# Performance work log

Measured on AMD Instinct MI355X. Metric: run time of the kernel, lower is better.

## Reference

```python
import jax, jax.numpy as jnp
import numpy as np

B, C, M = 2048, 1, 80  # M = max_object; matrices are (M+1)x(M+1)


def setup_inputs() -> dict:
    key = jax.random.key(0)
    k1, k2, k3, k4 = jax.random.split(key, 4)
    inp = {
        "input": jax.random.normal(k1, (B, C, M + 1, M + 1), dtype=jnp.float32),
        "target": jax.random.randint(k2, (B, C, M + 1, M + 1), 0, 2, dtype=jnp.int32),
        "mask0": jax.random.randint(k3, (B, C, M + 1), 0, 2, dtype=jnp.int32),
        "mask1": jax.random.randint(k4, (B, C, M + 1), 0, 2, dtype=jnp.int32),
        "outputs": 0,
        "current_fair_labels": 0,
        "next_fair_labels": 0,
    }
    return inp


def reference(input, target, mask0, mask1, outputs, current_fair_labels, next_fair_labels):
    f32 = jnp.float32
    m0 = mask0.astype(f32)[:, :, :, None]   # [B,C,M+1,1] (row mask, broadcast over cols)
    m1 = mask1.astype(f32)[:, :, None, :]   # [B,C,1,M+1] (col mask, broadcast over rows)
    mask_region = m0 * m1                    # [B,C,M+1,M+1]
    mask_region_pre = mask_region.at[:, :, M, :].set(0.0)   # zero last row
    mask_region_next = mask_region.at[:, :, :, M].set(0.0)  # zero last col
    mask_region_union = mask_region_pre * mask_region_next

    input_pre = jax.nn.softmax(mask_region_pre * input, axis=3)
    input_next = jax.nn.softmax(mask_region_next * input, axis=2)
    input_all = input_pre.at[:, :, :M, :M].set(
        jnp.maximum(input_pre, input_next)[:, :, :M, :M])

    t = target.astype(jnp.bool_).astype(f32)
    target_pre = mask_region_pre * t
    target_next = mask_region_next * t
    target_union = mask_region_union * t

    target_num = t.sum()
    n_pre = target_pre.sum()
    n_next = target_next.sum()
    n_union = target_union.sum()

    s_pre = -(target_pre * jnp.log(input_pre)).sum()
    loss_pre = jnp.where(n_pre > 0, s_pre / n_pre, s_pre)

    s_next = -(target_next * jnp.log(input_next)).sum()
    loss_next = jnp.where(n_next > 0, s_next / n_next, s_next)

    s_all = -(target_pre * jnp.log(input_all)).sum()
    loss = jnp.where((n_pre > 0) & (n_next > 0), s_all / n_pre, s_all)

    # |1 - p_pre - (1 - p_next)| == |p_next - p_pre|
    s_sim = (target_union * jnp.abs(input_next - input_pre)).sum()
    loss_similarity = jnp.where(n_union > 0, s_sim / target_num, s_sim)

    # accuracy on "pre" direction (argmax over cols, drop last row)
    idx_t_pre = jnp.argmax(target_pre, axis=3)[:, :, :-1]
    indexes_pre = jnp.argmax(input_all, axis=3)[:, :, :-1]
    mpre = mask0.astype(f32)[:, :, :-1]
    n_mpre = mpre.sum()
    s_acc_pre = ((indexes_pre == idx_t_pre).astype(f32) * mpre).sum()
    accuracy_pre = jnp.where(n_mpre > 0, s_acc_pre / n_mpre, s_acc_pre + 1.0)

    # accuracy on "next" direction (argmax over rows, drop last col)
    idx_t_next = jnp.argmax(target_next, axis=2)[:, :, :-1]
    indexes_next = jnp.argmax(input_next, axis=2)[:, :, :-1]
    mnext = mask1.astype(f32)[:, :, :-1]
    n_mnext = mnext.sum()
    s_acc_next = ((indexes_next == idx_t_next).astype(f32) * mnext).sum()
    accuracy_next = jnp.where(n_mnext > 0, s_acc_next / n_mnext, s_acc_next + 1.0)

    total = (loss_pre + loss_next + loss + loss_similarity) / 4.0
    return (loss_pre, loss_next, loss_similarity, total,
            accuracy_pre, accuracy_next, (accuracy_pre + accuracy_next) / 2.0,
            indexes_pre)
```

## Files before the change

### kernel.cpp

```cpp
#include <hip/hip_runtime.h>

#define M1 81
#define MSZ 80
#define NEL (M1 * M1)
#define NTW ((NEL + 31) / 32)
#define NACC 12


__device__ __forceinline__ float tbitf(const unsigned* tb, int idx) {
    return (float)((tb[idx >> 5] >> (idx & 31)) & 1u);
}

__global__ __launch_bounds__(256) void sst_main(
    const float* __restrict__ input,
    const int* __restrict__ target,
    const int* __restrict__ mask0,
    const int* __restrict__ mask1,
    float* __restrict__ out_idx,
    float* __restrict__ part,
    int slices)
{
    __shared__ float s_x[NEL];
    __shared__ unsigned s_tb[NTW];
    __shared__ float s_m0[M1], s_m1[M1];
    __shared__ float2 s_rowc[M1];
    __shared__ float4 s_colc[M1];
    __shared__ float s_pa[243];
    __shared__ float s_pv[243];
    __shared__ unsigned char s_pi[243];
    __shared__ unsigned char s_pt[243];
    __shared__ float s_accf[NACC];

    const int tid = threadIdx.x;
    const int slice = blockIdx.x;
    const size_t base = (size_t)slice * NEL;

    if (tid < NACC) s_accf[tid] = 0.0f;
    if (tid < M1) s_m0[tid] = (float)mask0[slice * M1 + tid];
    else if (tid >= 128 && tid < 128 + M1) s_m1[tid - 128] = (float)mask1[slice * M1 + (tid - 128)];

    for (int i = tid; i < NEL; i += 256) {
        s_x[i] = input[base + i];
        unsigned long long m = __ballot(target[base + i] != 0);
        if ((tid & 63) == 0) {
            int w = (i >> 5) & ~1;
            s_tb[w] = (unsigned)m;
            if (w + 1 < NTW) s_tb[w + 1] = (unsigned)(m >> 32);
        }
    }
    __syncthreads();

    float a[NACC];
#pragma unroll
    for (int k = 0; k < NACC; ++k) a[k] = 0.0f;

    const int g  = tid / 3;
    const int j  = tid - 3 * g;
    const int c0 = j * 27;
    const bool act = (tid < 243);

    if (act) {
        const int r = g;
        const float m0p = (r == MSZ) ? 0.0f : s_m0[r];
        const int rb = r * M1;
        float rs = 0.0f;
        for (int i = 0; i < 27; ++i) {
            const int c = c0 + i;
            rs += __expf(m0p * s_m1[c] * s_x[rb + c]);
        }
        s_pa[tid] = rs;
    }
    __syncthreads();
    if (tid < M1) {
        const float rsum = s_pa[3 * tid] + s_pa[3 * tid + 1] + s_pa[3 * tid + 2];
        s_rowc[tid] = make_float2(__logf(rsum), 1.0f / rsum);
    }
    __syncthreads();

    if (act) {
        const int c = g;
        const float mcol = (c == MSZ) ? 0.0f : s_m1[c];
        float cs = 0.0f, best = -1.0f;
        int bidx = c0, tIdxn = 127;
        for (int i = 0; i < 27; ++i) {
            const int r = c0 + i;
            const float mn = mcol * s_m0[r];
            const float e = __expf(mn * s_x[r * M1 + c]);
            cs += e;
            if (e > best) { best = e; bidx = r; }
            const float tn = tbitf(s_tb, r * M1 + c) * mn;
            if (tn != 0.0f && tIdxn == 127) tIdxn = r;
        }
        s_pa[tid] = cs;
        s_pv[tid] = best;
        s_pi[tid] = (unsigned char)bidx;
        s_pt[tid] = (unsigned char)tIdxn;
    }
    __syncthreads();
    if (tid < M1) {
        const int c = tid;
        const float csum = s_pa[3 * c] + s_pa[3 * c + 1] + s_pa[3 * c + 2];
        s_colc[c] = make_float4(s_m1[c], __logf(csum), 1.0f / csum, 0.0f);
        if (c < MSZ) {
            float bv = s_pv[3 * c]; int bi = s_pi[3 * c];
            float v1 = s_pv[3 * c + 1]; if (v1 > bv) { bv = v1; bi = s_pi[3 * c + 1]; }
            float v2 = s_pv[3 * c + 2]; if (v2 > bv) { bv = v2; bi = s_pi[3 * c + 2]; }
            int ti = min(min((int)s_pt[3 * c], (int)s_pt[3 * c + 1]), (int)s_pt[3 * c + 2]);
            if (ti == 127) ti = 0;
            const float m1c = s_m1[c];
            a[9]  += (bi == ti) ? m1c : 0.0f;
            a[11] += m1c;
        }
    }
    __syncthreads();

    if (act) {
        const int r = g;
        const int rb = r * M1;
        const float m0f = s_m0[r];
        const float m0p = (r == MSZ) ? 0.0f : m0f;
        const float2 rc = s_rowc[r];
        const float lr = rc.x, invr = rc.y;
        float bbest = -3.402823466e38f;
        int bbidx = c0, tIdx = 127;
        const int cend = (j == 2) ? MSZ : (c0 + 27);
        for (int c = c0; c < cend; ++c) {
            const float4 cc = s_colc[c];
            const float m1c = cc.x, kc = cc.y, invc = cc.z;
            const float x = s_x[rb + c];
            const float t = tbitf(s_tb, rb + c);
            const float mf = m0f * m1c;
            const float mp = m0p * m1c;
            const float z = mf * x;
            const float tp = t * mp;
            const float tn = t * mf;
            a[0] += t;
            a[1] += tp;
            a[2] += tn;
            a[3] += tp;
            a[4] = fmaf(tp, lr - z, a[4]);
            a[5] = fmaf(tn, kc - z, a[5]);
            const float mlk = fminf(lr, kc);
            a[6] = fmaf(tp, mlk - z, a[6]);
            const float e = __expf(z);
            a[7] = fmaf(tp * e, fabsf(invc - invr), a[7]);
            const float val = z - mlk;
            if (val > bbest) { bbest = val; bbidx = c; }
            if (tp != 0.0f && tIdx == 127) tIdx = c;
        }
        if (j == 2) {
            const int c = MSZ;
            const float m1c = s_m1[c];
            const float x = s_x[rb + c];
            const float t = tbitf(s_tb, rb + c);
            const float mp = m0p * m1c;
            const float zp = mp * x;
            const float tp = t * mp;
            a[0] += t;
            a[1] += tp;
            a[4] = fmaf(tp, lr - zp, a[4]);
            a[6] = fmaf(tp, lr - zp, a[6]);
            const float val = zp - lr;
            if (val > bbest) { bbest = val; bbidx = c; }
            if (tp != 0.0f && tIdx == 127) tIdx = c;
        }
        s_pv[tid] = bbest;
        s_pi[tid] = (unsigned char)bbidx;
        s_pt[tid] = (unsigned char)tIdx;
    }
    __syncthreads();

    if (tid < MSZ) {
        const int r = tid;
        float bv = s_pv[3 * r]; int bi = s_pi[3 * r];
        float v1 = s_pv[3 * r + 1]; if (v1 > bv) { bv = v1; bi = s_pi[3 * r + 1]; }
        float v2 = s_pv[3 * r + 2]; if (v2 > bv) { bv = v2; bi = s_pi[3 * r + 2]; }
        int ti = min(min((int)s_pt[3 * r], (int)s_pt[3 * r + 1]), (int)s_pt[3 * r + 2]);
        if (ti == 127) ti = 0;
        out_idx[(size_t)slice * MSZ + r] = (float)bi;
        const float m0r = s_m0[r];
        a[8]  += (bi == ti) ? m0r : 0.0f;
        a[10] += m0r;
    }

#pragma unroll
    for (int k = 0; k < NACC; ++k) {
        float v = a[k];
        for (int off = 32; off > 0; off >>= 1) v += __shfl_down(v, off);
        if ((tid & 63) == 0) atomicAdd(&s_accf[k], v);
    }
    __syncthreads();
    if (tid < NACC) part[(size_t)tid * slices + slice] = s_accf[tid];
}

__global__ __launch_bounds__(256) void sst_final(
    const float* __restrict__ part, int slices, float* __restrict__ out)
{
    __shared__ double s_part[4][NACC];
    const int tid = threadIdx.x;
    double l[NACC];
#pragma unroll
    for (int k = 0; k < NACC; ++k) l[k] = 0.0;
    for (int s = tid; s < slices; s += 256) {
#pragma unroll
        for (int k = 0; k < NACC; ++k) l[k] += (double)part[(size_t)k * slices + s];
    }
#pragma unroll
    for (int k = 0; k < NACC; ++k) {
        double v = l[k];
        for (int off = 32; off > 0; off >>= 1) v += __shfl_down(v, off);
        if ((tid & 63) == 0) s_part[tid >> 6][k] = v;
    }
    __syncthreads();
    if (tid == 0) {
        double g[NACC];
#pragma unroll
        for (int k = 0; k < NACC; ++k)
            g[k] = s_part[0][k] + s_part[1][k] + s_part[2][k] + s_part[3][k];
        const double tnum = g[0], npre = g[1], nnext = g[2], nunion = g[3];
        const double spre = g[4], snext = g[5], sall = g[6], ssim = g[7];
        const double accp = g[8], accn = g[9], nmp = g[10], nmn = g[11];
        const double loss_pre  = (npre > 0.0) ? spre / npre : spre;
        const double loss_next = (nnext > 0.0) ? snext / nnext : snext;
        const double loss      = (npre > 0.0 && nnext > 0.0) ? sall / npre : sall;
        const double loss_sim  = (nunion > 0.0) ? ssim / tnum : ssim;
        const double total = (loss_pre + loss_next + loss + loss_sim) * 0.25;
        const double ap = (nmp > 0.0) ? accp / nmp : accp + 1.0;
        const double an = (nmn > 0.0) ? accn / nmn : accn + 1.0;
        out[0] = (float)loss_pre;
        out[1] = (float)loss_next;
        out[2] = (float)loss_sim;
        out[3] = (float)total;
        out[4] = (float)ap;
        out[5] = (float)an;
        out[6] = (float)((ap + an) * 0.5);
    }
}

extern "C" void kernel_launch(void* const* d_in, const int* in_sizes, int n_in,
                              void* d_out, int out_size, void* d_ws, size_t ws_size,
                              hipStream_t stream) {
    const float* input  = (const float*)d_in[0];
    const int*   target = (const int*)d_in[1];
    const int*   mask0  = (const int*)d_in[2];
    const int*   mask1  = (const int*)d_in[3];
    float* out = (float*)d_out;
    float* part = (float*)d_ws;

    const int slices = in_sizes[0] / NEL;

    sst_main<<<slices, 256, 0, stream>>>(input, target, mask0, mask1, out + 7, part, slices);
    sst_final<<<1, 256, 0, stream>>>(part, slices, out);
}
```

Baseline: 183.3 us.

## Map rows to wavefronts with lane-per-column, reading global memory directly instead of staging in LDS

The per-slice kernel no longer stages the 81x81 input tile and a target bitmask in shared memory. Each wavefront now walks rows and each lane owns a column (two passes over global memory). Column softmax sums and argmaxes are kept in registers per lane, row sums are taken with wave shuffles, and the first-target row/column search uses ballots. This removes the LDS staging, the strided 3-threads-per-row layout and several barriers. In exchange input is read from global twice, lanes 17-63 sit idle in the second column chunk, and per-row shuffle reductions are added.

```diff
diff --git a/kernel.cpp b/kernel.cpp
--- a/kernel.cpp
+++ b/kernel.cpp
@@ -3,13 +3,9 @@
 #define M1 81
 #define MSZ 80
 #define NEL (M1 * M1)
-#define NTW ((NEL + 31) / 32)
 #define NACC 12
-
-
-__device__ __forceinline__ float tbitf(const unsigned* tb, int idx) {
-    return (float)((tb[idx >> 5] >> (idx & 31)) & 1u);
-}
+#define BIGKC 1.0e30f
+
 
 __global__ __launch_bounds__(256) void sst_main(
     const float* __restrict__ input,
@@ -20,174 +16,199 @@
     float* __restrict__ part,
     int slices)
 {
-    __shared__ float s_x[NEL];
-    __shared__ unsigned s_tb[NTW];
-    __shared__ float s_m0[M1], s_m1[M1];
-    __shared__ float2 s_rowc[M1];
-    __shared__ float4 s_colc[M1];
-    __shared__ float s_pa[243];
-    __shared__ float s_pv[243];
-    __shared__ unsigned char s_pi[243];
-    __shared__ unsigned char s_pt[243];
-    __shared__ float s_accf[NACC];
-
-    const int tid = threadIdx.x;
+    __shared__ float  s_m0[M1];
+    __shared__ float2 s_row[M1];
+    __shared__ float2 s_col[M1];
+    __shared__ float  s_cs[4][M1];
+    __shared__ float  s_cv[4][M1];
+    __shared__ int    s_ci[4][M1];
+    __shared__ int    s_ct[4][M1];
+    __shared__ float  s_accf[NACC];
+
+    const int tid   = threadIdx.x;
+    const int lane  = tid & 63;
+    const int w     = tid >> 6;
     const int slice = blockIdx.x;
     const size_t base = (size_t)slice * NEL;
 
     if (tid < NACC) s_accf[tid] = 0.0f;
     if (tid < M1) s_m0[tid] = (float)mask0[slice * M1 + tid];
-    else if (tid >= 128 && tid < 128 + M1) s_m1[tid - 128] = (float)mask1[slice * M1 + (tid - 128)];
-
-    for (int i = tid; i < NEL; i += 256) {
-        s_x[i] = input[base + i];
-        unsigned long long m = __ballot(target[base + i] != 0);
-        if ((tid & 63) == 0) {
-            int w = (i >> 5) & ~1;
-            s_tb[w] = (unsigned)m;
-            if (w + 1 < NTW) s_tb[w + 1] = (unsigned)(m >> 32);
-        }
-    }
-    __syncthreads();
+
+    const float m1c1 = (float)mask1[slice * M1 + lane];
+    float m1c2 = 0.0f;
+    if (lane < 17) m1c2 = (float)mask1[slice * M1 + 64 + lane];
+    const float m1n2 = (lane == 16) ? 0.0f : m1c2;
 
     float a[NACC];
 #pragma unroll
     for (int k = 0; k < NACC; ++k) a[k] = 0.0f;
 
-    const int g  = tid / 3;
-    const int j  = tid - 3 * g;
-    const int c0 = j * 27;
-    const bool act = (tid < 243);
-
-    if (act) {
-        const int r = g;
-        const float m0p = (r == MSZ) ? 0.0f : s_m0[r];
-        const int rb = r * M1;
-        float rs = 0.0f;
-        for (int i = 0; i < 27; ++i) {
-            const int c = c0 + i;
-            rs += __expf(m0p * s_m1[c] * s_x[rb + c]);
-        }
-        s_pa[tid] = rs;
-    }
-    __syncthreads();
-    if (tid < M1) {
-        const float rsum = s_pa[3 * tid] + s_pa[3 * tid + 1] + s_pa[3 * tid + 2];
-        s_rowc[tid] = make_float2(__logf(rsum), 1.0f / rsum);
-    }
-    __syncthreads();
-
-    if (act) {
-        const int c = g;
-        const float mcol = (c == MSZ) ? 0.0f : s_m1[c];
-        float cs = 0.0f, best = -1.0f;
-        int bidx = c0, tIdxn = 127;
-        for (int i = 0; i < 27; ++i) {
-            const int r = c0 + i;
-            const float mn = mcol * s_m0[r];
-            const float e = __expf(mn * s_x[r * M1 + c]);
-            cs += e;
-            if (e > best) { best = e; bidx = r; }
-            const float tn = tbitf(s_tb, r * M1 + c) * mn;
-            if (tn != 0.0f && tIdxn == 127) tIdxn = r;
-        }
-        s_pa[tid] = cs;
-        s_pv[tid] = best;
-        s_pi[tid] = (unsigned char)bidx;
-        s_pt[tid] = (unsigned char)tIdxn;
-    }
-    __syncthreads();
+    __syncthreads();
+
+    float csum1 = 0.0f, csum2 = 0.0f;
+    float cmv1 = -1.0f, cmv2 = -1.0f;
+    int   cmi1 = 0,     cmi2 = 0;
+
+    for (int r = w; r < M1; r += 4) {
+        const float m0f = s_m0[r];
+        const size_t rb = base + (size_t)r * M1;
+        const float x1 = input[rb + lane];
+        float x2 = 0.0f;
+        if (lane < 17) x2 = input[rb + 64 + lane];
+
+        if (r < MSZ) {
+            const float e1 = __expf(m0f * m1c1 * x1);
+            float e2 = 0.0f;
+            if (lane < 17) e2 = __expf(m0f * m1c2 * x2);
+            csum1 += e1;
+            if (e1 > cmv1) { cmv1 = e1; cmi1 = r; }
+            if (lane < 16) {
+                csum2 += e2;
+                if (e2 > cmv2) { cmv2 = e2; cmi2 = r; }
+            }
+            float s = e1 + e2;
+#pragma unroll
+            for (int off = 1; off < 64; off <<= 1) s += __shfl_xor(s, off);
+            if (lane == 0) s_row[r] = make_float2(__logf(s), 1.0f / s);
+        } else {
+            const float e1 = __expf(m0f * m1c1 * x1);
+            csum1 += e1;
+            if (e1 > cmv1) { cmv1 = e1; cmi1 = MSZ; }
+            if (lane < 16) {
+                const float e2 = __expf(m0f * m1c2 * x2);
+                csum2 += e2;
+                if (e2 > cmv2) { cmv2 = e2; cmi2 = MSZ; }
+            }
+            if (lane == 0) s_row[MSZ] = make_float2(__logf(81.0f), 1.0f / 81.0f);
+        }
+    }
+    s_cs[w][lane] = csum1;
+    s_cv[w][lane] = cmv1;
+    s_ci[w][lane] = cmi1;
+    if (lane < 16) {
+        s_cs[w][64 + lane] = csum2;
+        s_cv[w][64 + lane] = cmv2;
+        s_ci[w][64 + lane] = cmi2;
+    }
+    __syncthreads();
+
     if (tid < M1) {
         const int c = tid;
-        const float csum = s_pa[3 * c] + s_pa[3 * c + 1] + s_pa[3 * c + 2];
-        s_colc[c] = make_float4(s_m1[c], __logf(csum), 1.0f / csum, 0.0f);
         if (c < MSZ) {
-            float bv = s_pv[3 * c]; int bi = s_pi[3 * c];
-            float v1 = s_pv[3 * c + 1]; if (v1 > bv) { bv = v1; bi = s_pi[3 * c + 1]; }
-            float v2 = s_pv[3 * c + 2]; if (v2 > bv) { bv = v2; bi = s_pi[3 * c + 2]; }
-            int ti = min(min((int)s_pt[3 * c], (int)s_pt[3 * c + 1]), (int)s_pt[3 * c + 2]);
-            if (ti == 127) ti = 0;
-            const float m1c = s_m1[c];
-            a[9]  += (bi == ti) ? m1c : 0.0f;
-            a[11] += m1c;
-        }
-    }
-    __syncthreads();
-
-    if (act) {
-        const int r = g;
-        const int rb = r * M1;
+            const float csum = s_cs[0][c] + s_cs[1][c] + s_cs[2][c] + s_cs[3][c];
+            float bv = s_cv[0][c]; int bi = s_ci[0][c];
+#pragma unroll
+            for (int ww = 1; ww < 4; ++ww) {
+                const float v = s_cv[ww][c]; const int i = s_ci[ww][c];
+                if (v > bv || (v == bv && i < bi)) { bv = v; bi = i; }
+            }
+            s_ci[0][c] = bi;
+            s_col[c] = make_float2(__logf(csum), 1.0f / csum);
+        } else {
+            s_col[MSZ] = make_float2(BIGKC, 1.0f / 81.0f);
+        }
+    }
+    __syncthreads();
+
+    const float2 cc1 = s_col[lane];
+    const float kc1 = cc1.x, invc1 = cc1.y;
+    float kc2 = 0.0f, invc2 = 0.0f;
+    if (lane < 17) { const float2 cc2 = s_col[64 + lane]; kc2 = cc2.x; invc2 = cc2.y; }
+
+    int ct1 = 127, ct2 = 127;
+
+    for (int r = w; r < M1; r += 4) {
         const float m0f = s_m0[r];
-        const float m0p = (r == MSZ) ? 0.0f : m0f;
-        const float2 rc = s_rowc[r];
-        const float lr = rc.x, invr = rc.y;
-        float bbest = -3.402823466e38f;
-        int bbidx = c0, tIdx = 127;
-        const int cend = (j == 2) ? MSZ : (c0 + 27);
-        for (int c = c0; c < cend; ++c) {
-            const float4 cc = s_colc[c];
-            const float m1c = cc.x, kc = cc.y, invc = cc.z;
-            const float x = s_x[rb + c];
-            const float t = tbitf(s_tb, rb + c);
-            const float mf = m0f * m1c;
-            const float mp = m0p * m1c;
-            const float z = mf * x;
-            const float tp = t * mp;
-            const float tn = t * mf;
-            a[0] += t;
-            a[1] += tp;
-            a[2] += tn;
-            a[3] += tp;
-            a[4] = fmaf(tp, lr - z, a[4]);
-            a[5] = fmaf(tn, kc - z, a[5]);
-            const float mlk = fminf(lr, kc);
-            a[6] = fmaf(tp, mlk - z, a[6]);
-            const float e = __expf(z);
-            a[7] = fmaf(tp * e, fabsf(invc - invr), a[7]);
-            const float val = z - mlk;
-            if (val > bbest) { bbest = val; bbidx = c; }
-            if (tp != 0.0f && tIdx == 127) tIdx = c;
-        }
-        if (j == 2) {
-            const int c = MSZ;
-            const float m1c = s_m1[c];
-            const float x = s_x[rb + c];
-            const float t = tbitf(s_tb, rb + c);
-            const float mp = m0p * m1c;
-            const float zp = mp * x;
-            const float tp = t * mp;
-            a[0] += t;
-            a[1] += tp;
-            a[4] = fmaf(tp, lr - zp, a[4]);
-            a[6] = fmaf(tp, lr - zp, a[6]);
-            const float val = zp - lr;
-            if (val > bbest) { bbest = val; bbidx = c; }
-            if (tp != 0.0f && tIdx == 127) tIdx = c;
-        }
-        s_pv[tid] = bbest;
-        s_pi[tid] = (unsigned char)bbidx;
-        s_pt[tid] = (unsigned char)tIdx;
-    }
+        const bool last = (r == MSZ);
+        const float m0p = last ? 0.0f : m0f;
+        const float2 rw = s_row[r];
+        const float lr = rw.x, invr = rw.y;
+        const size_t rb = base + (size_t)r * M1;
+
+        const float x1 = input[rb + lane];
+        const int   t1 = target[rb + lane];
+        float x2 = 0.0f; int t2 = 0;
+        if (lane < 17) { x2 = input[rb + 64 + lane]; t2 = target[rb + 64 + lane]; }
+
+        const float tf1 = (t1 != 0) ? 1.0f : 0.0f;
+        const float mf1 = m0f * m1c1;
+        const float z1  = mf1 * x1;
+        const float mp1 = m0p * m1c1;
+        const float tp1 = tf1 * mp1;
+        const float tn1 = tf1 * mf1;
+        a[0] += tf1; a[1] += tp1; a[2] += tn1; a[3] += tp1;
+        a[4] = fmaf(tp1, lr - z1, a[4]);
+        a[5] = fmaf(tn1, kc1 - z1, a[5]);
+        const float mlk1 = fminf(lr, kc1);
+        a[6] = fmaf(tp1, mlk1 - z1, a[6]);
+        const float e1 = __expf(z1);
+        a[7] = fmaf(tp1 * e1, fabsf(invc1 - invr), a[7]);
+        float bv = z1 - mlk1; int bi = lane;
+        const bool tpnz1 = (tp1 != 0.0f);
+        if (tn1 != 0.0f && ct1 == 127) ct1 = r;
+
+        float val2 = -3.402823466e38f;
+        bool tpnz2 = false;
+        if (lane < 17) {
+            const float tf2 = (t2 != 0) ? 1.0f : 0.0f;
+            const float mf2 = m0f * m1c2;
+            const float z2  = mf2 * x2;
+            const float mp2 = m0p * m1c2;
+            const float tp2 = tf2 * mp2;
+            const float tn2 = tf2 * (m0f * m1n2);
+            const float tun2 = (lane == 16) ? 0.0f : tp2;
+            a[0] += tf2; a[1] += tp2; a[2] += tn2; a[3] += tun2;
+            a[4] = fmaf(tp2, lr - z2, a[4]);
+            a[5] = fmaf(tn2, kc2 - z2, a[5]);
+            const float mlk2 = fminf(lr, kc2);
+            a[6] = fmaf(tp2, mlk2 - z2, a[6]);
+            const float e2 = __expf(z2);
+            a[7] = fmaf(tun2 * e2, fabsf(invc2 - invr), a[7]);
+            val2 = z2 - mlk2;
+            tpnz2 = (tp2 != 0.0f);
+            if (tn2 != 0.0f && ct2 == 127) ct2 = r;
+        }
+
+        if (!last) {
+            if (val2 > bv) { bv = val2; bi = 64 + lane; }
+#pragma unroll
+            for (int off = 32; off > 0; off >>= 1) {
+                const float v2 = __shfl_down(bv, off);
+                const int   i2 = __shfl_down(bi, off);
+                if (v2 > bv || (v2 == bv && i2 < bi)) { bv = v2; bi = i2; }
+            }
+            const unsigned long long b1 = __ballot(tpnz1);
+            const unsigned long long b2 = __ballot(tpnz2);
+            if (lane == 0) {
+                int ti = 0;
+                if (b1) ti = __ffsll((long long)b1) - 1;
+                else if (b2) ti = 64 + __ffsll((long long)b2) - 1;
+                out_idx[(size_t)slice * MSZ + r] = (float)bi;
+                a[8]  += (bi == ti) ? m0f : 0.0f;
+                a[10] += m0f;
+            }
+        }
+    }
+
+    s_ct[w][lane] = ct1;
+    if (lane < 16) s_ct[w][64 + lane] = ct2;
     __syncthreads();
 
     if (tid < MSZ) {
-        const int r = tid;
-        float bv = s_pv[3 * r]; int bi = s_pi[3 * r];
-        float v1 = s_pv[3 * r + 1]; if (v1 > bv) { bv = v1; bi = s_pi[3 * r + 1]; }
-        float v2 = s_pv[3 * r + 2]; if (v2 > bv) { bv = v2; bi = s_pi[3 * r + 2]; }
-        int ti = min(min((int)s_pt[3 * r], (int)s_pt[3 * r + 1]), (int)s_pt[3 * r + 2]);
+        const int c = tid;
+        int ti = min(min(s_ct[0][c], s_ct[1][c]), min(s_ct[2][c], s_ct[3][c]));
         if (ti == 127) ti = 0;
-        out_idx[(size_t)slice * MSZ + r] = (float)bi;
-        const float m0r = s_m0[r];
-        a[8]  += (bi == ti) ? m0r : 0.0f;
-        a[10] += m0r;
+        const int bi = s_ci[0][c];
+        const float m1c = (float)mask1[slice * M1 + c];
+        a[9]  += (bi == ti) ? m1c : 0.0f;
+        a[11] += m1c;
     }
 
 #pragma unroll
     for (int k = 0; k < NACC; ++k) {
         float v = a[k];
         for (int off = 32; off > 0; off >>= 1) v += __shfl_down(v, off);
-        if ((tid & 63) == 0) atomicAdd(&s_accf[k], v);
+        if (lane == 0) atomicAdd(&s_accf[k], v);
     }
     __syncthreads();
     if (tid < NACC) part[(size_t)tid * slices + slice] = s_accf[tid];
```

After: 224.8 us. 22.6% more time.

## Split per-slice kernel into row/column stats and elementwise kernels with quad threads

Applied to the files above, without the earlier changes.

Replaces the one-block-per-slice kernel, which staged the input and a target bitmask in shared memory, with two grid-wide kernels. The first kernel computes row and column softmax statistics, the column argmax and the column target index, using four threads per row or column combined with cross-lane shuffles, and stores them in workspace. The second kernel does the elementwise loss and row argmax work. Both kernels read global memory directly and write per-block partial sums that the final kernel reduces. The aim is higher occupancy and more parallelism than the serial shared-memory phases allowed. The cost is reading input and target several times from global memory, with partly uncoalesced per-thread row segments.

```diff
diff --git a/kernel.cpp b/kernel.cpp
--- a/kernel.cpp
+++ b/kernel.cpp
@@ -3,141 +3,157 @@
 #define M1 81
 #define MSZ 80
 #define NEL (M1 * M1)
-#define NTW ((NEL + 31) / 32)
 #define NACC 12
-
-
-__device__ __forceinline__ float tbitf(const unsigned* tb, int idx) {
-    return (float)((tb[idx >> 5] >> (idx & 31)) & 1u);
-}
-
-__global__ __launch_bounds__(256) void sst_main(
+#define BIGKC 1.0e30f
+
+
+
+__device__ __forceinline__ void block_reduce_write(
+    float* a, float* part, int nbTot, int slot)
+{
+    __shared__ float s_wv[4][NACC];
+    const int tid = threadIdx.x;
+    const int lane = tid & 63, w = tid >> 6;
+#pragma unroll
+    for (int k = 0; k < NACC; ++k) {
+        float v = a[k];
+        for (int off = 32; off > 0; off >>= 1) v += __shfl_down(v, off);
+        if (lane == 0) s_wv[w][k] = v;
+    }
+    __syncthreads();
+    if (tid < NACC) {
+        part[tid * nbTot + slot] =
+            s_wv[0][tid] + s_wv[1][tid] + s_wv[2][tid] + s_wv[3][tid];
+    }
+}
+
+__global__ __launch_bounds__(256) void sst_stats(
     const float* __restrict__ input,
     const int* __restrict__ target,
     const int* __restrict__ mask0,
     const int* __restrict__ mask1,
+    float2* __restrict__ rowc,
+    float4* __restrict__ colc,
+    float* __restrict__ part, int nbTot, int slices, int rowBlocks)
+{
+    const int tid = threadIdx.x;
+    float a[NACC];
+#pragma unroll
+    for (int k = 0; k < NACC; ++k) a[k] = 0.0f;
+
+    if ((int)blockIdx.x < rowBlocks) {
+        const int t = blockIdx.x * 256 + tid;
+        if (t < slices * 324) {
+            const int slice = t / 324;
+            const int rem = t - slice * 324;
+            const int r = rem >> 2;
+            const int q = rem & 3;
+            const int mbase = slice * M1;
+            if (r == MSZ) {
+                if (q == 0) rowc[mbase + r] = make_float2(__logf(81.0f), 1.0f / 81.0f);
+            } else {
+                const float m0 = (float)mask0[mbase + r];
+                const size_t rb = (size_t)slice * NEL + (size_t)r * M1;
+                const int c0 = (q == 0) ? 0 : (20 * q + 1);
+                const int c1 = (q == 3) ? M1 : ((q == 0) ? 21 : c0 + 20);
+                float s = 0.0f;
+                for (int c = c0; c < c1; ++c) {
+                    const float m1c = (float)mask1[mbase + c];
+                    s += __expf(m0 * m1c * input[rb + c]);
+                }
+                s += __shfl_xor(s, 1);
+                s += __shfl_xor(s, 2);
+                if (q == 0) rowc[mbase + r] = make_float2(__logf(s), 1.0f / s);
+            }
+        }
+        return;
+    }
+
+    const int t = (blockIdx.x - rowBlocks) * 256 + tid;
+    if (t < slices * 324) {
+        const int slice = t / 324;
+        const int rem = t - slice * 324;
+        const int c = rem >> 2;
+        const int q = rem & 3;
+        const int mbase = slice * M1;
+        if (c == MSZ) {
+            if (q == 0) colc[mbase + c] =
+                make_float4((float)mask1[mbase + c], BIGKC, 1.0f / 81.0f, 0.0f);
+        } else {
+            const float m1c = (float)mask1[mbase + c];
+            const size_t sb = (size_t)slice * NEL;
+            const int r0 = (q == 0) ? 0 : (20 * q + 1);
+            const int r1 = (q == 0) ? 21 : (r0 + 20);
+            float cs = 0.0f, bv = -1.0f;
+            int bi = r0, ct = 127;
+            for (int r = r0; r < r1; ++r) {
+                const float m0r = (float)mask0[mbase + r];
+                const float mn = m1c * m0r;
+                const float e = __expf(mn * input[sb + (size_t)r * M1 + c]);
+                cs += e;
+                if (e > bv) { bv = e; bi = r; }
+                if (ct == 127 && mn != 0.0f && target[sb + (size_t)r * M1 + c] != 0) ct = r;
+            }
+            cs += __shfl_xor(cs, 1);
+            cs += __shfl_xor(cs, 2);
+            float ov = __shfl_xor(bv, 1); int oi = __shfl_xor(bi, 1); int ot = __shfl_xor(ct, 1);
+            if (ov > bv || (ov == bv && oi < bi)) { bv = ov; bi = oi; }
+            ct = min(ct, ot);
+            ov = __shfl_xor(bv, 2); oi = __shfl_xor(bi, 2); ot = __shfl_xor(ct, 2);
+            if (ov > bv || (ov == bv && oi < bi)) { bv = ov; bi = oi; }
+            ct = min(ct, ot);
+            if (q == 0) {
+                colc[mbase + c] = make_float4(m1c, __logf(cs), 1.0f / cs, 0.0f);
+                const int ti = (ct == 127) ? 0 : ct;
+                a[9]  += (bi == ti) ? m1c : 0.0f;
+                a[11] += m1c;
+            }
+        }
+    }
+    block_reduce_write(a, part, nbTot, blockIdx.x - rowBlocks);
+}
+
+__global__ __launch_bounds__(256) void sst_elem(
+    const float* __restrict__ input,
+    const int* __restrict__ target,
+    const int* __restrict__ mask0,
+    const float2* __restrict__ rowc,
+    const float4* __restrict__ colc,
     float* __restrict__ out_idx,
-    float* __restrict__ part,
-    int slices)
-{
-    __shared__ float s_x[NEL];
-    __shared__ unsigned s_tb[NTW];
-    __shared__ float s_m0[M1], s_m1[M1];
-    __shared__ float2 s_rowc[M1];
-    __shared__ float4 s_colc[M1];
-    __shared__ float s_pa[243];
-    __shared__ float s_pv[243];
-    __shared__ unsigned char s_pi[243];
-    __shared__ unsigned char s_pt[243];
-    __shared__ float s_accf[NACC];
-
-    const int tid = threadIdx.x;
-    const int slice = blockIdx.x;
-    const size_t base = (size_t)slice * NEL;
-
-    if (tid < NACC) s_accf[tid] = 0.0f;
-    if (tid < M1) s_m0[tid] = (float)mask0[slice * M1 + tid];
-    else if (tid >= 128 && tid < 128 + M1) s_m1[tid - 128] = (float)mask1[slice * M1 + (tid - 128)];
-
-    for (int i = tid; i < NEL; i += 256) {
-        s_x[i] = input[base + i];
-        unsigned long long m = __ballot(target[base + i] != 0);
-        if ((tid & 63) == 0) {
-            int w = (i >> 5) & ~1;
-            s_tb[w] = (unsigned)m;
-            if (w + 1 < NTW) s_tb[w + 1] = (unsigned)(m >> 32);
-        }
-    }
-    __syncthreads();
-
+    float* __restrict__ part, int nbTot, int partBase, int slices)
+{
+    const int tid = threadIdx.x;
     float a[NACC];
 #pragma unroll
     for (int k = 0; k < NACC; ++k) a[k] = 0.0f;
 
-    const int g  = tid / 3;
-    const int j  = tid - 3 * g;
-    const int c0 = j * 27;
-    const bool act = (tid < 243);
-
-    if (act) {
-        const int r = g;
-        const float m0p = (r == MSZ) ? 0.0f : s_m0[r];
-        const int rb = r * M1;
-        float rs = 0.0f;
-        for (int i = 0; i < 27; ++i) {
-            const int c = c0 + i;
-            rs += __expf(m0p * s_m1[c] * s_x[rb + c]);
-        }
-        s_pa[tid] = rs;
-    }
-    __syncthreads();
-    if (tid < M1) {
-        const float rsum = s_pa[3 * tid] + s_pa[3 * tid + 1] + s_pa[3 * tid + 2];
-        s_rowc[tid] = make_float2(__logf(rsum), 1.0f / rsum);
-    }
-    __syncthreads();
-
-    if (act) {
-        const int c = g;
-        const float mcol = (c == MSZ) ? 0.0f : s_m1[c];
-        float cs = 0.0f, best = -1.0f;
-        int bidx = c0, tIdxn = 127;
-        for (int i = 0; i < 27; ++i) {
-            const int r = c0 + i;
-            const float mn = mcol * s_m0[r];
-            const float e = __expf(mn * s_x[r * M1 + c]);
-            cs += e;
-            if (e > best) { best = e; bidx = r; }
-            const float tn = tbitf(s_tb, r * M1 + c) * mn;
-            if (tn != 0.0f && tIdxn == 127) tIdxn = r;
-        }
-        s_pa[tid] = cs;
-        s_pv[tid] = best;
-        s_pi[tid] = (unsigned char)bidx;
-        s_pt[tid] = (unsigned char)tIdxn;
-    }
-    __syncthreads();
-    if (tid < M1) {
-        const int c = tid;
-        const float csum = s_pa[3 * c] + s_pa[3 * c + 1] + s_pa[3 * c + 2];
-        s_colc[c] = make_float4(s_m1[c], __logf(csum), 1.0f / csum, 0.0f);
-        if (c < MSZ) {
-            float bv = s_pv[3 * c]; int bi = s_pi[3 * c];
-            float v1 = s_pv[3 * c + 1]; if (v1 > bv) { bv = v1; bi = s_pi[3 * c + 1]; }
-            float v2 = s_pv[3 * c + 2]; if (v2 > bv) { bv = v2; bi = s_pi[3 * c + 2]; }
-            int ti = min(min((int)s_pt[3 * c], (int)s_pt[3 * c + 1]), (int)s_pt[3 * c + 2]);
-            if (ti == 127) ti = 0;
-            const float m1c = s_m1[c];
-            a[9]  += (bi == ti) ? m1c : 0.0f;
-            a[11] += m1c;
-        }
-    }
-    __syncthreads();
-
-    if (act) {
-        const int r = g;
-        const int rb = r * M1;
-        const float m0f = s_m0[r];
+    const int t = blockIdx.x * 256 + tid;
+    if (t < slices * 324) {
+        const int slice = t / 324;
+        const int rem = t - slice * 324;
+        const int r = rem >> 2;
+        const int q = rem & 3;
+        const int mbase = slice * M1;
+        const size_t rb = (size_t)slice * NEL + (size_t)r * M1;
+        const float m0f = (float)mask0[mbase + r];
         const float m0p = (r == MSZ) ? 0.0f : m0f;
-        const float2 rc = s_rowc[r];
-        const float lr = rc.x, invr = rc.y;
-        float bbest = -3.402823466e38f;
-        int bbidx = c0, tIdx = 127;
-        const int cend = (j == 2) ? MSZ : (c0 + 27);
-        for (int c = c0; c < cend; ++c) {
-            const float4 cc = s_colc[c];
+        const float2 rw = rowc[mbase + r];
+        const float lr = rw.x, invr = rw.y;
+        const int c0 = (q == 0) ? 0 : (20 * q + 1);
+        const int c1 = (q == 3) ? MSZ : ((q == 0) ? 21 : c0 + 20);
+        float bv = -3.402823466e38f;
+        int bi = c0, ti = 127;
+        for (int c = c0; c < c1; ++c) {
+            const float4 cc = colc[mbase + c];
             const float m1c = cc.x, kc = cc.y, invc = cc.z;
-            const float x = s_x[rb + c];
-            const float t = tbitf(s_tb, rb + c);
+            const float x = input[rb + c];
+            const float tf = (target[rb + c] != 0) ? 1.0f : 0.0f;
             const float mf = m0f * m1c;
+            const float z  = mf * x;
             const float mp = m0p * m1c;
-            const float z = mf * x;
-            const float tp = t * mp;
-            const float tn = t * mf;
-            a[0] += t;
-            a[1] += tp;
-            a[2] += tn;
-            a[3] += tp;
+            const float tp = tf * mp;
+            const float tn = tf * mf;
+            a[0] += tf; a[1] += tp; a[2] += tn; a[3] += tp;
             a[4] = fmaf(tp, lr - z, a[4]);
             a[5] = fmaf(tn, kc - z, a[5]);
             const float mlk = fminf(lr, kc);
@@ -145,65 +161,50 @@
             const float e = __expf(z);
             a[7] = fmaf(tp * e, fabsf(invc - invr), a[7]);
             const float val = z - mlk;
-            if (val > bbest) { bbest = val; bbidx = c; }
-            if (tp != 0.0f && tIdx == 127) tIdx = c;
-        }
-        if (j == 2) {
-            const int c = MSZ;
-            const float m1c = s_m1[c];
-            const float x = s_x[rb + c];
-            const float t = tbitf(s_tb, rb + c);
-            const float mp = m0p * m1c;
-            const float zp = mp * x;
-            const float tp = t * mp;
-            a[0] += t;
-            a[1] += tp;
-            a[4] = fmaf(tp, lr - zp, a[4]);
-            a[6] = fmaf(tp, lr - zp, a[6]);
-            const float val = zp - lr;
-            if (val > bbest) { bbest = val; bbidx = c; }
-            if (tp != 0.0f && tIdx == 127) tIdx = c;
-        }
-        s_pv[tid] = bbest;
-        s_pi[tid] = (unsigned char)bbidx;
-        s_pt[tid] = (unsigned char)tIdx;
-    }
-    __syncthreads();
-
-    if (tid < MSZ) {
-        const int r = tid;
-        float bv = s_pv[3 * r]; int bi = s_pi[3 * r];
-        float v1 = s_pv[3 * r + 1]; if (v1 > bv) { bv = v1; bi = s_pi[3 * r + 1]; }
-        float v2 = s_pv[3 * r + 2]; if (v2 > bv) { bv = v2; bi = s_pi[3 * r + 2]; }
-        int ti = min(min((int)s_pt[3 * r], (int)s_pt[3 * r + 1]), (int)s_pt[3 * r + 2]);
-        if (ti == 127) ti = 0;
-        out_idx[(size_t)slice * MSZ + r] = (float)bi;
-        const float m0r = s_m0[r];
-        a[8]  += (bi == ti) ? m0r : 0.0f;
-        a[10] += m0r;
-    }
-
-#pragma unroll
-    for (int k = 0; k < NACC; ++k) {
-        float v = a[k];
-        for (int off = 32; off > 0; off >>= 1) v += __shfl_down(v, off);
-        if ((tid & 63) == 0) atomicAdd(&s_accf[k], v);
-    }
-    __syncthreads();
-    if (tid < NACC) part[(size_t)tid * slices + slice] = s_accf[tid];
+            if (val > bv) { bv = val; bi = c; }
+            if (ti == 127 && tp != 0.0f) ti = c;
+        }
+        if (q == 3) {
+            const float4 cc = colc[mbase + MSZ];
+            const float m1c = cc.x;
+            const float x = input[rb + MSZ];
+            const float tf = (target[rb + MSZ] != 0) ? 1.0f : 0.0f;
+            const float z  = m0f * m1c * x;
+            const float tp = tf * (m0p * m1c);
+            a[0] += tf; a[1] += tp;
+            a[4] = fmaf(tp, lr - z, a[4]);
+            a[6] = fmaf(tp, lr - z, a[6]);
+            const float val = z - lr;
+            if (val > bv) { bv = val; bi = MSZ; }
+            if (ti == 127 && tp != 0.0f) ti = MSZ;
+        }
+        float ov = __shfl_xor(bv, 1); int oi = __shfl_xor(bi, 1); int ot = __shfl_xor(ti, 1);
+        if (ov > bv || (ov == bv && oi < bi)) { bv = ov; bi = oi; }
+        ti = min(ti, ot);
+        ov = __shfl_xor(bv, 2); oi = __shfl_xor(bi, 2); ot = __shfl_xor(ti, 2);
+        if (ov > bv || (ov == bv && oi < bi)) { bv = ov; bi = oi; }
+        ti = min(ti, ot);
+        if (q == 0 && r < MSZ) {
+            out_idx[(size_t)slice * MSZ + r] = (float)bi;
+            const int tm = (ti == 127) ? 0 : ti;
+            a[8]  += (bi == tm) ? m0f : 0.0f;
+            a[10] += m0f;
+        }
+    }
+    block_reduce_write(a, part, nbTot, partBase + blockIdx.x);
 }
 
 __global__ __launch_bounds__(256) void sst_final(
-    const float* __restrict__ part, int slices, float* __restrict__ out)
+    const float* __restrict__ part, int nbTot, float* __restrict__ out)
 {
     __shared__ double s_part[4][NACC];
     const int tid = threadIdx.x;
     double l[NACC];
 #pragma unroll
     for (int k = 0; k < NACC; ++k) l[k] = 0.0;
-    for (int s = tid; s < slices; s += 256) {
-#pragma unroll
-        for (int k = 0; k < NACC; ++k) l[k] += (double)part[(size_t)k * slices + s];
+    for (int s = tid; s < nbTot; s += 256) {
+#pragma unroll
+        for (int k = 0; k < NACC; ++k) l[k] += (double)part[(size_t)k * nbTot + s];
     }
 #pragma unroll
     for (int k = 0; k < NACC; ++k) {
@@ -245,10 +246,19 @@
     const int*   mask0  = (const int*)d_in[2];
     const int*   mask1  = (const int*)d_in[3];
     float* out = (float*)d_out;
-    float* part = (float*)d_ws;
 
     const int slices = in_sizes[0] / NEL;
-
-    sst_main<<<slices, 256, 0, stream>>>(input, target, mask0, mask1, out + 7, part, slices);
-    sst_final<<<1, 256, 0, stream>>>(part, slices, out);
-}
+    const int qBlocks = (slices * 324 + 255) / 256;
+    const int k1Blocks = qBlocks * 2;
+    const int nbTot = qBlocks * 2;
+
+    float4* colc = (float4*)d_ws;
+    float2* rowc = (float2*)(colc + (size_t)slices * M1);
+    float*  part = (float*)(rowc + (size_t)slices * M1);
+
+    sst_stats<<<k1Blocks, 256, 0, stream>>>(input, target, mask0, mask1,
+                                            rowc, colc, part, nbTot, slices, qBlocks);
+    sst_elem<<<qBlocks, 256, 0, stream>>>(input, target, mask0,
+                                          rowc, colc, out + 7, part, nbTot, qBlocks, slices);
+    sst_final<<<1, 256, 0, stream>>>(part, nbTot, out);
+}
```

Measured after the change: 313.0 us. +70.8%, slower.

## Run row and column softmax passes concurrently with 512-thread blocks and algebraic loss split

Applied to the files above, without the earlier changes.

Raises the block to 512 threads so the row-sum pass and the column-sum pass run in parallel on separate thread groups instead of in two serialized phases. The log-softmax terms are split algebraically: target-weighted z sums and target counts are accumulated in the first pass and combined with log-sums afterwards, and the target-index searches move into that pass. The final pass uses six threads per row. Per-wave partials go to a shared array instead of shared atomics. This removes one sync phase and shortens per-thread loops, at the cost of more shared memory, more registers per block, and reordered floating-point sums.

```diff
diff --git a/kernel.cpp b/kernel.cpp
--- a/kernel.cpp
+++ b/kernel.cpp
@@ -5,13 +5,16 @@
 #define NEL (M1 * M1)
 #define NTW ((NEL + 31) / 32)
 #define NACC 12
+#define BIGKC 1.0e30f
+#define LOG81 4.394449154672439f
+#define INV81 0.012345679012345678f
 
 
 __device__ __forceinline__ float tbitf(const unsigned* tb, int idx) {
     return (float)((tb[idx >> 5] >> (idx & 31)) & 1u);
 }
 
-__global__ __launch_bounds__(256) void sst_main(
+__global__ __launch_bounds__(512, 8) void sst_main(
     const float* __restrict__ input,
     const int* __restrict__ target,
     const int* __restrict__ mask0,
@@ -25,172 +28,198 @@
     __shared__ float s_m0[M1], s_m1[M1];
     __shared__ float2 s_rowc[M1];
     __shared__ float4 s_colc[M1];
-    __shared__ float s_pa[243];
-    __shared__ float s_pv[243];
-    __shared__ unsigned char s_pi[243];
-    __shared__ unsigned char s_pt[243];
-    __shared__ float s_accf[NACC];
-
-    const int tid = threadIdx.x;
+    __shared__ float s_pA[486];
+    __shared__ float s_pB[486];
+    __shared__ float s_pV[486];
+    __shared__ unsigned char s_pI[486];
+    __shared__ unsigned char s_pT[486];
+    __shared__ unsigned char s_ti[M1];
+    __shared__ float s_wv[8][NACC];
+
+    const int tid   = threadIdx.x;
+    const int lane  = tid & 63;
+    const int w     = tid >> 6;
     const int slice = blockIdx.x;
     const size_t base = (size_t)slice * NEL;
 
-    if (tid < NACC) s_accf[tid] = 0.0f;
     if (tid < M1) s_m0[tid] = (float)mask0[slice * M1 + tid];
     else if (tid >= 128 && tid < 128 + M1) s_m1[tid - 128] = (float)mask1[slice * M1 + (tid - 128)];
 
-    for (int i = tid; i < NEL; i += 256) {
+    float a[NACC];
+#pragma unroll
+    for (int k = 0; k < NACC; ++k) a[k] = 0.0f;
+
+    for (int i = tid; i < NEL; i += 512) {
         s_x[i] = input[base + i];
-        unsigned long long m = __ballot(target[base + i] != 0);
-        if ((tid & 63) == 0) {
-            int w = (i >> 5) & ~1;
-            s_tb[w] = (unsigned)m;
-            if (w + 1 < NTW) s_tb[w + 1] = (unsigned)(m >> 32);
-        }
-    }
-    __syncthreads();
-
-    float a[NACC];
-#pragma unroll
-    for (int k = 0; k < NACC; ++k) a[k] = 0.0f;
-
-    const int g  = tid / 3;
-    const int j  = tid - 3 * g;
-    const int c0 = j * 27;
-    const bool act = (tid < 243);
-
-    if (act) {
-        const int r = g;
-        const float m0p = (r == MSZ) ? 0.0f : s_m0[r];
-        const int rb = r * M1;
-        float rs = 0.0f;
-        for (int i = 0; i < 27; ++i) {
-            const int c = c0 + i;
-            rs += __expf(m0p * s_m1[c] * s_x[rb + c]);
-        }
-        s_pa[tid] = rs;
-    }
-    __syncthreads();
+        const int tv = target[base + i];
+        a[0] += (tv != 0) ? 1.0f : 0.0f;
+        unsigned long long m = __ballot(tv != 0);
+        if (lane == 0) {
+            const int w2 = (i >> 5) & ~1;
+            s_tb[w2] = (unsigned)m;
+            if (w2 + 1 < NTW) s_tb[w2 + 1] = (unsigned)(m >> 32);
+        }
+    }
+    __syncthreads();
+
+    if (tid < 243) {
+        const int r = tid / 3, j = tid - 3 * (tid / 3);
+        if (r < MSZ) {
+            const float m0p = s_m0[r];
+            const int rb = r * M1;
+            const int c0 = 27 * j;
+            float rs = 0.0f, St = 0.0f, Sz = 0.0f;
+            int ti = 127;
+            for (int c = c0; c < c0 + 27; ++c) {
+                const float m1c = s_m1[c];
+                const float x = s_x[rb + c];
+                const float mp = m0p * m1c;
+                const float z = mp * x;
+                rs += __expf(z);
+                const float tf = tbitf(s_tb, rb + c);
+                const float tp = tf * mp;
+                a[1] += tp;
+                a[3] += (c < MSZ) ? tp : 0.0f;
+                Sz = fmaf(tp, z, Sz);
+                St += tp;
+                if (ti == 127 && tp != 0.0f) ti = c;
+            }
+            a[4] -= Sz;
+            a[6] -= Sz;
+            s_pA[tid] = rs;
+            s_pB[tid] = St;
+            s_pT[tid] = (unsigned char)ti;
+        }
+    } else if (tid >= 256 && tid < 499) {
+        const int u = tid - 256;
+        const int c = u / 3, j = u - 3 * (u / 3);
+        if (c < MSZ) {
+            const float m1n = s_m1[c];
+            const int r0 = 27 * j;
+            float cs = 0.0f, Sn = 0.0f, Sz = 0.0f, bv = -1.0f;
+            int bi = r0, ct = 127;
+            for (int r = r0; r < r0 + 27; ++r) {
+                const float mn = m1n * s_m0[r];
+                const float x = s_x[r * M1 + c];
+                const float z = mn * x;
+                const float e = __expf(z);
+                cs += e;
+                if (e > bv) { bv = e; bi = r; }
+                const float tf = tbitf(s_tb, r * M1 + c);
+                const float tn = tf * mn;
+                a[2] += tn;
+                Sz = fmaf(tn, z, Sz);
+                Sn += tn;
+                if (ct == 127 && tn != 0.0f) ct = r;
+            }
+            a[5] -= Sz;
+            s_pA[243 + u] = cs;
+            s_pB[243 + u] = Sn;
+            s_pV[243 + u] = bv;
+            s_pI[243 + u] = (unsigned char)bi;
+            s_pT[243 + u] = (unsigned char)ct;
+        }
+    }
+    __syncthreads();
+
     if (tid < M1) {
-        const float rsum = s_pa[3 * tid] + s_pa[3 * tid + 1] + s_pa[3 * tid + 2];
-        s_rowc[tid] = make_float2(__logf(rsum), 1.0f / rsum);
-    }
-    __syncthreads();
-
-    if (act) {
-        const int c = g;
-        const float mcol = (c == MSZ) ? 0.0f : s_m1[c];
-        float cs = 0.0f, best = -1.0f;
-        int bidx = c0, tIdxn = 127;
-        for (int i = 0; i < 27; ++i) {
-            const int r = c0 + i;
-            const float mn = mcol * s_m0[r];
-            const float e = __expf(mn * s_x[r * M1 + c]);
-            cs += e;
-            if (e > best) { best = e; bidx = r; }
-            const float tn = tbitf(s_tb, r * M1 + c) * mn;
-            if (tn != 0.0f && tIdxn == 127) tIdxn = r;
-        }
-        s_pa[tid] = cs;
-        s_pv[tid] = best;
-        s_pi[tid] = (unsigned char)bidx;
-        s_pt[tid] = (unsigned char)tIdxn;
-    }
-    __syncthreads();
-    if (tid < M1) {
-        const int c = tid;
-        const float csum = s_pa[3 * c] + s_pa[3 * c + 1] + s_pa[3 * c + 2];
-        s_colc[c] = make_float4(s_m1[c], __logf(csum), 1.0f / csum, 0.0f);
+        const int r = tid;
+        if (r < MSZ) {
+            const int b = 3 * r;
+            const float rs = s_pA[b] + s_pA[b + 1] + s_pA[b + 2];
+            const float lr = __logf(rs);
+            s_rowc[r] = make_float2(lr, 1.0f / rs);
+            const float St = s_pB[b] + s_pB[b + 1] + s_pB[b + 2];
+            a[4] = fmaf(St, lr, a[4]);
+            int ti = min(min((int)s_pT[b], (int)s_pT[b + 1]), (int)s_pT[b + 2]);
+            s_ti[r] = (unsigned char)((ti == 127) ? 0 : ti);
+        } else {
+            s_rowc[r] = make_float2(LOG81, INV81);
+            s_ti[r] = 0;
+        }
+    } else if (tid >= 128 && tid < 128 + M1) {
+        const int c = tid - 128;
         if (c < MSZ) {
-            float bv = s_pv[3 * c]; int bi = s_pi[3 * c];
-            float v1 = s_pv[3 * c + 1]; if (v1 > bv) { bv = v1; bi = s_pi[3 * c + 1]; }
-            float v2 = s_pv[3 * c + 2]; if (v2 > bv) { bv = v2; bi = s_pi[3 * c + 2]; }
-            int ti = min(min((int)s_pt[3 * c], (int)s_pt[3 * c + 1]), (int)s_pt[3 * c + 2]);
-            if (ti == 127) ti = 0;
+            const int b = 243 + 3 * c;
+            const float cs = s_pA[b] + s_pA[b + 1] + s_pA[b + 2];
+            const float kc = __logf(cs);
             const float m1c = s_m1[c];
-            a[9]  += (bi == ti) ? m1c : 0.0f;
+            s_colc[c] = make_float4(m1c, kc, 1.0f / cs, 0.0f);
+            const float Sn = s_pB[b] + s_pB[b + 1] + s_pB[b + 2];
+            a[5] = fmaf(Sn, kc, a[5]);
+            float bv = s_pV[b]; int bi = s_pI[b];
+            const float v1 = s_pV[b + 1]; if (v1 > bv) { bv = v1; bi = s_pI[b + 1]; }
+            const float v2 = s_pV[b + 2]; if (v2 > bv) { bv = v2; bi = s_pI[b + 2]; }
+            int ct = min(min((int)s_pT[b], (int)s_pT[b + 1]), (int)s_pT[b + 2]);
+            if (ct == 127) ct = 0;
+            a[9]  += (bi == ct) ? m1c : 0.0f;
             a[11] += m1c;
-        }
-    }
-    __syncthreads();
-
-    if (act) {
-        const int r = g;
+        } else {
+            s_colc[c] = make_float4(s_m1[c], BIGKC, INV81, 0.0f);
+        }
+    }
+    __syncthreads();
+
+    if (tid < 486) {
+        const int r = tid / 6, j2 = tid - 6 * (tid / 6);
+        const int c0 = j2 * 13 + ((j2 < 3) ? j2 : 3);
+        const int c1 = c0 + ((j2 < 3) ? 14 : 13);
         const int rb = r * M1;
         const float m0f = s_m0[r];
         const float m0p = (r == MSZ) ? 0.0f : m0f;
-        const float2 rc = s_rowc[r];
-        const float lr = rc.x, invr = rc.y;
-        float bbest = -3.402823466e38f;
-        int bbidx = c0, tIdx = 127;
-        const int cend = (j == 2) ? MSZ : (c0 + 27);
-        for (int c = c0; c < cend; ++c) {
+        const float2 rw = s_rowc[r];
+        const float lr = rw.x, invr = rw.y;
+        float bv = -3.402823466e38f;
+        int bi = c0;
+        for (int c = c0; c < c1; ++c) {
             const float4 cc = s_colc[c];
             const float m1c = cc.x, kc = cc.y, invc = cc.z;
             const float x = s_x[rb + c];
-            const float t = tbitf(s_tb, rb + c);
+            const float tf = tbitf(s_tb, rb + c);
             const float mf = m0f * m1c;
+            const float z = mf * x;
+            const float mlk = fminf(lr, kc);
             const float mp = m0p * m1c;
-            const float z = mf * x;
-            const float tp = t * mp;
-            const float tn = t * mf;
-            a[0] += t;
-            a[1] += tp;
-            a[2] += tn;
-            a[3] += tp;
-            a[4] = fmaf(tp, lr - z, a[4]);
-            a[5] = fmaf(tn, kc - z, a[5]);
-            const float mlk = fminf(lr, kc);
-            a[6] = fmaf(tp, mlk - z, a[6]);
+            const float tp = tf * mp;
+            a[6] = fmaf(tp, mlk, a[6]);
             const float e = __expf(z);
-            a[7] = fmaf(tp * e, fabsf(invc - invr), a[7]);
+            const float t7 = (c < MSZ) ? tp : 0.0f;
+            a[7] = fmaf(t7 * e, fabsf(invc - invr), a[7]);
             const float val = z - mlk;
-            if (val > bbest) { bbest = val; bbidx = c; }
-            if (tp != 0.0f && tIdx == 127) tIdx = c;
-        }
-        if (j == 2) {
-            const int c = MSZ;
-            const float m1c = s_m1[c];
-            const float x = s_x[rb + c];
-            const float t = tbitf(s_tb, rb + c);
-            const float mp = m0p * m1c;
-            const float zp = mp * x;
-            const float tp = t * mp;
-            a[0] += t;
-            a[1] += tp;
-            a[4] = fmaf(tp, lr - zp, a[4]);
-            a[6] = fmaf(tp, lr - zp, a[6]);
-            const float val = zp - lr;
-            if (val > bbest) { bbest = val; bbidx = c; }
-            if (tp != 0.0f && tIdx == 127) tIdx = c;
-        }
-        s_pv[tid] = bbest;
-        s_pi[tid] = (unsigned char)bbidx;
-        s_pt[tid] = (unsigned char)tIdx;
+            if (val > bv) { bv = val; bi = c; }
+        }
+        s_pV[tid] = bv;
+        s_pI[tid] = (unsigned char)bi;
     }
     __syncthreads();
 
     if (tid < MSZ) {
-        const int r = tid;
-        float bv = s_pv[3 * r]; int bi = s_pi[3 * r];
-        float v1 = s_pv[3 * r + 1]; if (v1 > bv) { bv = v1; bi = s_pi[3 * r + 1]; }
-        float v2 = s_pv[3 * r + 2]; if (v2 > bv) { bv = v2; bi = s_pi[3 * r + 2]; }
-        int ti = min(min((int)s_pt[3 * r], (int)s_pt[3 * r + 1]), (int)s_pt[3 * r + 2]);
-        if (ti == 127) ti = 0;
+        const int r = tid, b = 6 * r;
+        float bv = s_pV[b]; int bi = s_pI[b];
+#pragma unroll
+        for (int k = 1; k < 6; ++k) {
+            const float v = s_pV[b + k];
+            if (v > bv) { bv = v; bi = s_pI[b + k]; }
+        }
         out_idx[(size_t)slice * MSZ + r] = (float)bi;
-        const float m0r = s_m0[r];
-        a[8]  += (bi == ti) ? m0r : 0.0f;
-        a[10] += m0r;
+        const float m0f = s_m0[r];
+        a[8]  += (bi == (int)s_ti[r]) ? m0f : 0.0f;
+        a[10] += m0f;
     }
 
 #pragma unroll
     for (int k = 0; k < NACC; ++k) {
         float v = a[k];
         for (int off = 32; off > 0; off >>= 1) v += __shfl_down(v, off);
-        if ((tid & 63) == 0) atomicAdd(&s_accf[k], v);
-    }
-    __syncthreads();
-    if (tid < NACC) part[(size_t)tid * slices + slice] = s_accf[tid];
+        if (lane == 0) s_wv[w][k] = v;
+    }
+    __syncthreads();
+    if (tid < NACC) {
+        float s = 0.0f;
+#pragma unroll
+        for (int ww = 0; ww < 8; ++ww) s += s_wv[ww][tid];
+        part[(size_t)tid * slices + slice] = s;
+    }
 }
 
 __global__ __launch_bounds__(256) void sst_final(
@@ -249,6 +278,6 @@
 
     const int slices = in_sizes[0] / NEL;
 
-    sst_main<<<slices, 256, 0, stream>>>(input, target, mask0, mask1, out + 7, part, slices);
+    sst_main<<<slices, 512, 0, stream>>>(input, target, mask0, mask1, out + 7, part, slices);
     sst_final<<<1, 256, 0, stream>>>(part, slices, out);
 }
```

After: 170.2 us. 7.1% less time.
